# Kernel optimization log

Hardware: AMD Instinct MI355X
Metric: run time of the kernel (lower is better)

The kernel has to match this reference:

```python
import jax, jax.numpy as jnp
import numpy as np

S, D, H, HD = 3072, 1280, 16, 80
FF = 4 * D
EPS = 1e-6


def layernorm(x, scale, bias):
    mu = jnp.mean(x, axis=-1, keepdims=True)
    var = jnp.mean(jnp.square(x - mu), axis=-1, keepdims=True)
    return (x - mu) * jax.lax.rsqrt(var + EPS) * scale + bias


def rotate_half(x):
    x1 = x[..., : x.shape[-1] // 2]
    x2 = x[..., x.shape[-1] // 2 :]
    return jnp.concatenate([-x2, x1], axis=-1)


def apply_rope(x, freqs):
    # x: (S,H,hd), freqs: (S,hd/2)
    cos = jnp.repeat(jnp.cos(freqs), 2, axis=-1)[:, None, :]  # (S,1,hd)
    sin = jnp.repeat(jnp.sin(freqs), 2, axis=-1)[:, None, :]
    return x * cos + rotate_half(x) * sin


def quick_gelu(x):
    return x * jax.nn.sigmoid(1.702 * x)


def setup_inputs() -> dict:
    key = jax.random.key(0)
    ks = jax.random.split(key, 12)
    s = 0.02
    return {
        "hidden_states": jax.random.normal(ks[0], (S, D), jnp.float32),
        "rotary_pos_emb": jax.random.normal(ks[1], (S, HD // 2), jnp.float32),
        "ln1_scale": jnp.ones((D,), jnp.float32),
        "ln1_bias": jnp.zeros((D,), jnp.float32),
        "ln2_scale": jnp.ones((D,), jnp.float32),
        "ln2_bias": jnp.zeros((D,), jnp.float32),
        "qkv_w": jax.random.normal(ks[2], (D, 3 * D), jnp.float32) * s,
        "qkv_b": jnp.zeros((3 * D,), jnp.float32),
        "proj_w": jax.random.normal(ks[3], (D, D), jnp.float32) * s,
        "proj_b": jnp.zeros((D,), jnp.float32),
        "fc1_w": jax.random.normal(ks[4], (D, FF), jnp.float32) * s,
        "fc1_b": jnp.zeros((FF,), jnp.float32),
        "fc2_w": jax.random.normal(ks[5], (FF, D), jnp.float32) * s,
        "fc2_b": jnp.zeros((D,), jnp.float32),
        "cu_seqlens": jnp.array([0, 1024, 2048, 3072], jnp.int32),
    }


def reference(hidden_states, rotary_pos_emb, ln1_scale, ln1_bias, ln2_scale,
              ln2_bias, qkv_w, qkv_b, proj_w, proj_b, fc1_w, fc1_b, fc2_w,
              fc2_b, cu_seqlens):
    x = hidden_states  # (S, D)
    h = layernorm(x, ln1_scale, ln1_bias)
    qkv = (h @ qkv_w + qkv_b).reshape(S, 3, H, HD)
    q, k, v = qkv[:, 0], qkv[:, 1], qkv[:, 2]  # each (S, H, hd)
    q = apply_rope(q, rotary_pos_emb)
    k = apply_rope(k, rotary_pos_emb)

    # block-diagonal varlen mask from cu_seqlens (same segment attends)
    ids = jnp.arange(S)
    seg = jnp.searchsorted(cu_seqlens, ids, side="right")  # (S,)
    valid = seg[:, None] == seg[None, :]  # (S, S)
    bias = jnp.where(valid, 0.0, jnp.finfo(q.dtype).min)

    scale = 1.0 / jnp.sqrt(jnp.asarray(HD, q.dtype))
    scores = jnp.einsum("qhd,khd->hqk", q, k) * scale + bias
    probs = jax.nn.softmax(scores.astype(jnp.float32), axis=-1).astype(q.dtype)
    attn = jnp.einsum("hqk,khd->qhd", probs, v).reshape(S, D)
    attn = attn @ proj_w + proj_b

    x = x + attn
    h2 = layernorm(x, ln2_scale, ln2_bias)
    mlp = quick_gelu(h2 @ fc1_w + fc1_b) @ fc2_w + fc2_b
    return x + mlp
```

## Files before the change

### kernel.cpp

```cpp
#include <hip/hip_runtime.h>

typedef __bf16 bf16x8 __attribute__((ext_vector_type(8)));
typedef float f32x4 __attribute__((ext_vector_type(4)));
typedef unsigned short u16;
typedef u16 u16x4 __attribute__((ext_vector_type(4)));
typedef u16 u16x8 __attribute__((ext_vector_type(8)));
typedef float float4v __attribute__((ext_vector_type(4)));

__device__ __forceinline__ u16 f2bf(float f) {
    __bf16 b = (__bf16)f;
    return __builtin_bit_cast(unsigned short, b);
}
__device__ __forceinline__ float bf2f(u16 x) {
    __bf16 b = __builtin_bit_cast(__bf16, x);
    return (float)b;
}

__device__ __forceinline__ void gld16(const void* g, void* l) {
    __builtin_amdgcn_global_load_lds((const __attribute__((address_space(1))) void*)g,
                                     (__attribute__((address_space(3))) void*)l, 16, 0, 0);
}

__device__ __forceinline__ int xcd_swz(int orig, int nwg) {
    const int q = nwg >> 3, r = nwg & 7;
    const int xcd = orig & 7, pos = orig >> 3;
    return (xcd < r ? xcd * (q + 1) : r * (q + 1) + (xcd - r) * q) + pos;
}

__global__ __launch_bounds__(256) void transpose_all_kernel(
    const float* __restrict__ qkvw, const float* __restrict__ projw,
    const float* __restrict__ fc1w, const float* __restrict__ fc2w,
    u16* __restrict__ qkvwT, u16* __restrict__ projwT,
    u16* __restrict__ fc1wT, u16* __restrict__ fc2wT)
{
    __shared__ u16 tile[64][65];
    int bid = blockIdx.x;
    const float* W; u16* WT; int K, N, nx;
    if (bid < 1200)      { W = qkvw;  WT = qkvwT;  K = 1280; N = 3840; nx = 60; }
    else if (bid < 1600) { bid -= 1200; W = projw; WT = projwT; K = 1280; N = 1280; nx = 20; }
    else if (bid < 3200) { bid -= 1600; W = fc1w;  WT = fc1wT;  K = 1280; N = 5120; nx = 80; }
    else                 { bid -= 3200; W = fc2w;  WT = fc2wT;  K = 5120; N = 1280; nx = 20; }
    const int tx = threadIdx.x & 63, ty = threadIdx.x >> 6;
    const int n0 = (bid % nx) * 64, k0 = (bid / nx) * 64;
    #pragma unroll
    for (int i = ty; i < 64; i += 4)
        tile[i][tx] = f2bf(W[(size_t)(k0 + i) * N + n0 + tx]);
    __syncthreads();
    #pragma unroll
    for (int i = ty; i < 64; i += 4)
        WT[(size_t)(n0 + i) * K + k0 + tx] = tile[tx][i];
}

__global__ __launch_bounds__(256) void ln_kernel(
    const float* __restrict__ x, const float* __restrict__ sc,
    const float* __restrict__ bias, u16* __restrict__ out)
{
    const int row = blockIdx.x, t = threadIdx.x;
    const float* xr = x + (size_t)row * 1280;
    float v[5], s1 = 0.f, s2 = 0.f;
    #pragma unroll
    for (int i = 0; i < 5; i++) {
        v[i] = xr[t + i * 256];
        s1 += v[i];
        s2 += v[i] * v[i];
    }
    #pragma unroll
    for (int off = 32; off; off >>= 1) {
        s1 += __shfl_down(s1, off);
        s2 += __shfl_down(s2, off);
    }
    __shared__ float rA[4], rB[4];
    if ((t & 63) == 0) { rA[t >> 6] = s1; rB[t >> 6] = s2; }
    __syncthreads();
    s1 = rA[0] + rA[1] + rA[2] + rA[3];
    s2 = rB[0] + rB[1] + rB[2] + rB[3];
    const float mu = s1 * (1.f / 1280.f);
    const float var = s2 * (1.f / 1280.f) - mu * mu;
    const float rstd = rsqrtf(var + 1e-6f);
    #pragma unroll
    for (int i = 0; i < 5; i++) {
        const int d = t + i * 256;
        out[(size_t)row * 1280 + d] = f2bf((v[i] - mu) * rstd * sc[d] + bias[d]);
    }
}

__global__ __launch_bounds__(256) void reduce4_ln_kernel(
    const u16* __restrict__ parts, const float* __restrict__ bias,
    const float* __restrict__ res, const float* __restrict__ lns,
    const float* __restrict__ lnb, float* __restrict__ xmid,
    u16* __restrict__ h2, size_t MN)
{
    const int row = blockIdx.x, t = threadIdx.x;
    float v[5], s1 = 0.f, s2 = 0.f;
    #pragma unroll
    for (int i = 0; i < 5; i++) {
        const int d = t + i * 256;
        const size_t idx = (size_t)row * 1280 + d;
        float a = bf2f(parts[idx]) + bf2f(parts[MN + idx])
                + bf2f(parts[2 * MN + idx]) + bf2f(parts[3 * MN + idx])
                + res[idx] + bias[d];
        v[i] = a;
        xmid[idx] = a;
        s1 += a;
        s2 += a * a;
    }
    #pragma unroll
    for (int off = 32; off; off >>= 1) {
        s1 += __shfl_down(s1, off);
        s2 += __shfl_down(s2, off);
    }
    __shared__ float rA[4], rB[4];
    if ((t & 63) == 0) { rA[t >> 6] = s1; rB[t >> 6] = s2; }
    __syncthreads();
    s1 = rA[0] + rA[1] + rA[2] + rA[3];
    s2 = rB[0] + rB[1] + rB[2] + rB[3];
    const float mu = s1 * (1.f / 1280.f);
    const float var = s2 * (1.f / 1280.f) - mu * mu;
    const float rstd = rsqrtf(var + 1e-6f);
    #pragma unroll
    for (int i = 0; i < 5; i++) {
        const int d = t + i * 256;
        h2[(size_t)row * 1280 + d] = f2bf((v[i] - mu) * rstd * lns[d] + lnb[d]);
    }
}

__global__ __launch_bounds__(256) void reduce4b_kernel(
    const u16* __restrict__ parts, const float* __restrict__ bias,
    const float* __restrict__ res, float* __restrict__ out, int N, size_t MN)
{
    const size_t i4 = ((size_t)blockIdx.x * 256 + threadIdx.x) * 4;
    if (i4 >= MN) return;
    float4v a = *reinterpret_cast<const float4v*>(res + i4);
    #pragma unroll
    for (int p = 0; p < 4; p++) {
        u16x4 v = *reinterpret_cast<const u16x4*>(parts + p * MN + i4);
        #pragma unroll
        for (int r = 0; r < 4; r++) a[r] += bf2f(v[r]);
    }
    const int col = (int)(i4 % N);
    a += *reinterpret_cast<const float4v*>(bias + col);
    *reinterpret_cast<float4v*>(out + i4) = a;
}

template <int GELU, int OUTB, int SPLIT>
__global__ __launch_bounds__(512, 2) void gemm256_kernel(
    const u16* __restrict__ A, const u16* __restrict__ BT,
    const float* __restrict__ bias,
    float* __restrict__ outF, u16* __restrict__ outB,
    int M, int N, int K)
{
    __shared__ u16 As[2][256 * 64];
    __shared__ u16 Bs[2][256 * 64];
    const int tid = threadIdx.x, lane = tid & 63, wave = tid >> 6;
    const int nwg = gridDim.x * gridDim.y;
    const int bid = xcd_swz(blockIdx.y * gridDim.x + blockIdx.x, nwg);
    const int m0 = (bid / gridDim.x) * 256, n0 = (bid % gridDim.x) * 256;
    const int wr = wave >> 2, wc = wave & 3;
    const int wm = wr * 128, wn = wc * 64;
    const int lr = lane & 15, lh = lane >> 4;
    const int xa = lr & 7;

    const int kchunk = K / SPLIT;
    const int kz = (SPLIT > 1) ? blockIdx.z : 0;
    const int kbeg = kz * kchunk;
    const int niter = kchunk >> 7;

    const int sr = lane >> 3;
    const int sc8 = (lane & 7) ^ sr;

    f32x4 acc[8][4] = {};
    bf16x8 bq[4][2];

    const char* aRd[2] = {
        (const char*)As + (wm + lr) * 128 + ((0 + lh) ^ xa) * 16,
        (const char*)As + (wm + lr) * 128 + ((4 + lh) ^ xa) * 16 };
    const char* bRd[2] = {
        (const char*)Bs + (wn + lr) * 128 + ((0 + lh) ^ xa) * 16,
        (const char*)Bs + (wn + lr) * 128 + ((4 + lh) ^ xa) * 16 };

    const u16 *aG[2][2], *bG[2][2];
    #pragma unroll
    for (int h = 0; h < 2; h++)
        #pragma unroll
        for (int j = 0; j < 2; j++) {
            const int row = h * 128 + j * 64 + wave * 8 + sr;
            aG[h][j] = A + (size_t)(m0 + row) * K + kbeg + sc8 * 8;
            bG[h][j] = BT + (size_t)(n0 + row) * K + kbeg + sc8 * 8;
        }

    auto stgA = [&](int t, int h) {
        u16* d = (u16*)As + (t & 1) * 16384 + h * 8192 + wave * 512;
        gld16(aG[h][0] + (size_t)t * 64, d);
        gld16(aG[h][1] + (size_t)t * 64, d + 4096);
    };
    auto stgB = [&](int t, int h) {
        u16* d = (u16*)Bs + (t & 1) * 16384 + h * 8192 + wave * 512;
        gld16(bG[h][0] + (size_t)t * 64, d);
        gld16(bG[h][1] + (size_t)t * 64, d + 4096);
    };

#define PHASE(BUF, Q, STGSTMT, VMSTMT)                                          \
    {                                                                           \
        if ((Q) == 0) {                                                         \
            _Pragma("unroll") for (int ni = 0; ni < 4; ni++)                    \
                _Pragma("unroll") for (int kk = 0; kk < 2; kk++)                \
                    bq[ni][kk] = *reinterpret_cast<const bf16x8*>(              \
                        bRd[kk] + (BUF) * 32768 + ni * 2048);                   \
        }                                                                       \
        bf16x8 afq[2][2];                                                       \
        _Pragma("unroll") for (int m2 = 0; m2 < 2; m2++)                        \
            _Pragma("unroll") for (int kk = 0; kk < 2; kk++)                    \
                afq[m2][kk] = *reinterpret_cast<const bf16x8*>(                 \
                    aRd[kk] + (BUF) * 32768 + (Q) * 4096 + m2 * 2048);          \
        VMSTMT;                                                                 \
        __builtin_amdgcn_s_barrier();                                           \
        asm volatile("s_waitcnt lgkmcnt(0)" ::: "memory");                      \
        __builtin_amdgcn_s_setprio(1);                                          \
        _Pragma("unroll") for (int kk = 0; kk < 2; kk++)                        \
            _Pragma("unroll") for (int m2 = 0; m2 < 2; m2++)                    \
                _Pragma("unroll") for (int ni = 0; ni < 4; ni++)                \
                    acc[(Q) * 2 + m2][ni] =                                     \
                        __builtin_amdgcn_mfma_f32_16x16x32_bf16(                \
                            afq[m2][kk], bq[ni][kk], acc[(Q) * 2 + m2][ni],     \
                            0, 0, 0);                                           \
        __builtin_amdgcn_s_setprio(0);                                          \
        STGSTMT;                                                                \
    }

    stgB(0, 0); stgB(0, 1);
    stgA(0, 0); stgA(0, 1);
    stgB(1, 0); stgB(1, 1);
    asm volatile("s_waitcnt vmcnt(4)" ::: "memory");
    __builtin_amdgcn_s_barrier();

    for (int i = 0; i < niter - 1; i++) {
        const int t0 = 2 * i, t1 = 2 * i + 1;
        PHASE(0, 0, stgA(t1, 0), (void)0);
        PHASE(0, 1, stgA(t1, 1), (void)0);
        PHASE(0, 2, stgB(t0 + 2, 0), (void)0);
        PHASE(0, 3, stgB(t0 + 2, 1),
              asm volatile("s_waitcnt vmcnt(2)" ::: "memory"));
        PHASE(1, 0, stgA(t0 + 2, 0), (void)0);
        PHASE(1, 1, stgA(t0 + 2, 1), (void)0);
        PHASE(1, 2, stgB(t1 + 2, 0), (void)0);
        PHASE(1, 3, stgB(t1 + 2, 1),
              asm volatile("s_waitcnt vmcnt(2)" ::: "memory"));
    }
    {
        const int t1 = 2 * niter - 1;
        PHASE(0, 0, stgA(t1, 0), (void)0);
        PHASE(0, 1, stgA(t1, 1), (void)0);
        PHASE(0, 2, (void)0, (void)0);
        PHASE(0, 3, (void)0,
              asm volatile("s_waitcnt vmcnt(0)" ::: "memory"));
        PHASE(1, 0, (void)0, (void)0);
        PHASE(1, 1, (void)0, (void)0);
        PHASE(1, 2, (void)0, (void)0);
        PHASE(1, 3, (void)0, (void)0);
    }
#undef PHASE

    if (SPLIT > 1) {
        u16* pf = outB + (size_t)kz * M * N;
        #pragma unroll
        for (int mi = 0; mi < 8; mi++)
            #pragma unroll
            for (int ni = 0; ni < 4; ni++) {
                const int col = n0 + wn + ni * 16 + lr;
                #pragma unroll
                for (int r = 0; r < 4; r++) {
                    const int rowg = m0 + wm + mi * 16 + lh * 4 + r;
                    pf[(size_t)rowg * N + col] = f2bf(acc[mi][ni][r]);
                }
            }
        return;
    }

    #pragma unroll
    for (int mi = 0; mi < 8; mi++) {
        #pragma unroll
        for (int ni = 0; ni < 4; ni++) {
            const int col = n0 + wn + ni * 16 + lr;
            const float bv = bias[col];
            #pragma unroll
            for (int r = 0; r < 4; r++) {
                const int rowg = m0 + wm + mi * 16 + lh * 4 + r;
                float v = acc[mi][ni][r] + bv;
                if (GELU) v = v * (1.0f / (1.0f + __expf(-1.702f * v)));
                if (OUTB) outB[(size_t)rowg * N + col] = f2bf(v);
            }
        }
    }
}

template <int SPLIT>
__global__ __launch_bounds__(256) void gemm_kernel(
    const u16* __restrict__ A, const u16* __restrict__ BT,
    u16* __restrict__ partB, int M, int N, int K)
{
    __shared__ u16 As[128 * 64];
    __shared__ u16 Bs[128 * 64];
    const int tid = threadIdx.x, lane = tid & 63, wave = tid >> 6;
    const int nwg = gridDim.x * gridDim.y;
    const int bid = xcd_swz(blockIdx.y * gridDim.x + blockIdx.x, nwg);
    const int m0 = (bid / gridDim.x) * 128, n0 = (bid % gridDim.x) * 128;
    const int wm = (wave >> 1) * 64, wn = (wave & 1) * 64;
    const int lr = lane & 15, lh = lane >> 4;
    const int xa = lr & 7;
    const int srow = lane >> 3;
    const int schunk = (lane & 7) ^ (srow & 7);

    const int kchunk = K / SPLIT;
    const int kz = (SPLIT > 1) ? blockIdx.z : 0;
    const int kbeg = kz * kchunk;

    const u16 *aG[4], *bG[4];
    u16 *dA[4], *dB[4];
    #pragma unroll
    for (int s = 0; s < 4; s++) {
        const int seg = wave + s * 4;
        const int row = seg * 8 + srow;
        aG[s] = A + (size_t)(m0 + row) * K + kbeg + schunk * 8;
        bG[s] = BT + (size_t)(n0 + row) * K + kbeg + schunk * 8;
        dA[s] = As + seg * 512;
        dB[s] = Bs + seg * 512;
    }
    const char* aRd[2] = {
        (const char*)As + (wm + lr) * 128 + ((0 + lh) ^ xa) * 16,
        (const char*)As + (wm + lr) * 128 + ((4 + lh) ^ xa) * 16 };
    const char* bRd[2] = {
        (const char*)Bs + (wn + lr) * 128 + ((0 + lh) ^ xa) * 16,
        (const char*)Bs + (wn + lr) * 128 + ((4 + lh) ^ xa) * 16 };

    f32x4 acc[4][4] = {};

    for (int ko = 0; ko < kchunk; ko += 64) {
        #pragma unroll
        for (int s = 0; s < 4; s++) {
            gld16(aG[s] + ko, dA[s]);
            gld16(bG[s] + ko, dB[s]);
        }
        asm volatile("s_waitcnt vmcnt(0)" ::: "memory");
        __syncthreads();

        bf16x8 af[4][2], bfr[4][2];
        #pragma unroll
        for (int mi = 0; mi < 4; mi++)
            #pragma unroll
            for (int kk = 0; kk < 2; kk++)
                af[mi][kk] = *reinterpret_cast<const bf16x8*>(aRd[kk] + mi * 2048);
        #pragma unroll
        for (int ni = 0; ni < 4; ni++)
            #pragma unroll
            for (int kk = 0; kk < 2; kk++)
                bfr[ni][kk] = *reinterpret_cast<const bf16x8*>(bRd[kk] + ni * 2048);
        #pragma unroll
        for (int kk = 0; kk < 2; kk++)
            #pragma unroll
            for (int mi = 0; mi < 4; mi++)
                #pragma unroll
                for (int ni = 0; ni < 4; ni++)
                    acc[mi][ni] = __builtin_amdgcn_mfma_f32_16x16x32_bf16(
                        af[mi][kk], bfr[ni][kk], acc[mi][ni], 0, 0, 0);
        __syncthreads();
    }

    u16* pf = partB + (size_t)kz * M * N;
    #pragma unroll
    for (int mi = 0; mi < 4; mi++)
        #pragma unroll
        for (int ni = 0; ni < 4; ni++) {
            const int col = n0 + wn + ni * 16 + lr;
            #pragma unroll
            for (int r = 0; r < 4; r++) {
                const int rowg = m0 + wm + mi * 16 + lh * 4 + r;
                pf[(size_t)rowg * N + col] = f2bf(acc[mi][ni][r]);
            }
        }
}

__global__ __launch_bounds__(256) void rope_kernel(
    const u16* __restrict__ qkv, const float* __restrict__ freqs,
    u16* __restrict__ qp, u16* __restrict__ kp, u16* __restrict__ vt)
{
    const int s = blockIdx.x, t = threadIdx.x;
    const float scale = 0.1118033988749895f;
    __shared__ float cs[40], sn[40];
    if (t < 40) {
        const float f = freqs[(size_t)s * 40 + t];
        cs[t] = cosf(f);
        sn[t] = sinf(f);
    }
    __syncthreads();
    const u16* row = qkv + (size_t)s * 3840;
    for (int i = t; i < 1280; i += 256) {
        const int h = i / 80, d = i % 80;
        const float c = cs[d >> 1], sv = sn[d >> 1];
        const float q0 = bf2f(row[i]);
        const float q1 = (d < 40) ? -bf2f(row[i + 40]) : bf2f(row[i - 40]);
        qp[((size_t)h * 3072 + s) * 96 + d] = f2bf((q0 * c + q1 * sv) * scale);
        const float k0 = bf2f(row[1280 + i]);
        const float k1 = (d < 40) ? -bf2f(row[1280 + i + 40]) : bf2f(row[1280 + i - 40]);
        kp[((size_t)h * 3072 + s) * 128 + d] = f2bf(k0 * c + k1 * sv);
        vt[((size_t)h * 80 + d) * 3072 + s] = row[2560 + i];
    }
    {
        const int h = t / 16, d = 80 + (t % 16);
        qp[((size_t)h * 3072 + s) * 96 + d] = 0;
    }
    for (int i = t; i < 768; i += 256) {
        const int h = i / 48, d = 80 + (i % 48);
        kp[((size_t)h * 3072 + s) * 128 + d] = 0;
    }
}

__global__ __launch_bounds__(256) void attn_kernel(
    const u16* __restrict__ qp, const u16* __restrict__ kp,
    const u16* __restrict__ vt, u16* __restrict__ attn_out)
{
    const int tid = threadIdx.x, lane = tid & 63, wave = tid >> 6;
    const int w = xcd_swz(blockIdx.x, 768);
    const int qt = w & 15;
    const int h = (w >> 4) & 15;
    const int sq = w >> 8;
    const int lr = lane & 15, lh = lane >> 4;
    const int xa = lr & 7;
    const int qrow = sq * 1024 + qt * 64 + wave * 16;

    __shared__ u16 Ks[2][64 * 128];
    __shared__ u16 Vs[2][80 * 64];

    bf16x8 aq[3];
    {
        const u16* qb = qp + ((size_t)h * 3072 + qrow + lr) * 96 + lh * 8;
        #pragma unroll
        for (int d0 = 0; d0 < 3; d0++)
            aq[d0] = *reinterpret_cast<const bf16x8*>(qb + d0 * 32);
    }

    float m = -1e30f, l = 0.f;
    f32x4 acc[5] = {};

    const u16* kseg = kp + ((size_t)h * 3072 + sq * 1024) * 128;
    const u16* vseg = vt + (size_t)h * 80 * 3072 + sq * 1024;

    const int krow_l = lane >> 4;
    const int kch    = lane & 15;
    const int vrow_l = lane >> 3;
    const int vch    = lane & 7;

    const u16 *kG[4], *vG[3];
    u16 *kD[4], *vD[3];
    #pragma unroll
    for (int s = 0; s < 4; s++) {
        const int seg = wave + s * 4;
        const int row = seg * 4 + krow_l;
        kG[s] = kseg + (size_t)row * 128 + ((kch ^ (row & 7)) * 8);
        kD[s] = (u16*)Ks + seg * 512;
    }
    #pragma unroll
    for (int s = 0; s < 3; s++) {
        const int seg = wave + s * 4;
        const int row = (seg < 10) ? seg * 8 + vrow_l : 0;
        vG[s] = vseg + (size_t)row * 3072 + ((vch ^ (row & 7)) * 8);
        vD[s] = (u16*)Vs + seg * 512;
    }

    auto stageK = [&](int t, int buf) {
        #pragma unroll
        for (int s = 0; s < 4; s++)
            gld16(kG[s] + (size_t)t * 8192, kD[s] + buf * 8192);
    };
    auto stageV = [&](int t, int buf) {
        #pragma unroll
        for (int s = 0; s < 3; s++)
            if (wave + s * 4 < 10)
                gld16(vG[s] + t * 64, vD[s] + buf * 5120);
    };

    stageK(0, 0);
    stageV(0, 0);
    asm volatile("s_waitcnt vmcnt(0)" ::: "memory");
    __syncthreads();

    const char* kRd[3] = {
        (const char*)Ks + lr * 256 + ((0 + lh) ^ xa) * 16,
        (const char*)Ks + lr * 256 + ((4 + lh) ^ xa) * 16,
        (const char*)Ks + lr * 256 + ((8 + lh) ^ xa) * 16 };
    const char* vRd[2] = {
        (const char*)Vs + lr * 128 + ((0 + lh) ^ xa) * 16,
        (const char*)Vs + lr * 128 + ((4 + lh) ^ xa) * 16 };

    const int prow = wave * 16 + lr;
    const int psw = prow & 7;
    const char* pBase = (const char*)Ks + prow * 256;
    const int prd = ((12 + lh) ^ psw) << 4;

    for (int t = 0; t < 16; t++) {
        const int cur = t & 1;
        const int curK = cur * 16384, curV = cur * 10240;
        if (t < 15) {
            stageK(t + 1, cur ^ 1);
            stageV(t + 1, cur ^ 1);
        }

        f32x4 sc[4] = {};
        #pragma unroll
        for (int c = 0; c < 4; c++) {
            #pragma unroll
            for (int d0 = 0; d0 < 3; d0++) {
                bf16x8 kf = *reinterpret_cast<const bf16x8*>(kRd[d0] + curK + c * 4096);
                sc[c] = __builtin_amdgcn_mfma_f32_16x16x32_bf16(kf, aq[d0], sc[c], 0, 0, 0);
            }
        }

        float pmax = sc[0][0];
        #pragma unroll
        for (int c = 0; c < 4; c++)
            #pragma unroll
            for (int r = 0; r < 4; r++)
                pmax = fmaxf(pmax, sc[c][r]);
        pmax = fmaxf(pmax, __shfl_xor(pmax, 16));
        pmax = fmaxf(pmax, __shfl_xor(pmax, 32));

        if (!__all(pmax - m <= 8.0f)) {
            const float mn = fmaxf(m, pmax);
            const float fac = __expf(m - mn);
            m = mn;
            l *= fac;
            #pragma unroll
            for (int df = 0; df < 5; df++)
                #pragma unroll
                for (int r = 0; r < 4; r++)
                    acc[df][r] *= fac;
        }

        float p[4][4], rs = 0.f;
        #pragma unroll
        for (int c = 0; c < 4; c++)
            #pragma unroll
            for (int r = 0; r < 4; r++) {
                p[c][r] = __expf(sc[c][r] - m);
                rs += p[c][r];
            }
        rs += __shfl_xor(rs, 16);
        rs += __shfl_xor(rs, 32);
        l += rs;

        char* pb = (char*)pBase + curK;

        #pragma unroll
        for (int cc = 0; cc < 2; cc++) {
            u16x4 pw;
            #pragma unroll
            for (int r = 0; r < 4; r++)
                pw[r] = f2bf(p[cc][r]);
            *reinterpret_cast<u16x4*>(
                pb + (((12 + cc * 2 + (lh >> 1)) ^ psw) << 4) + (lh & 1) * 8) = pw;
        }
        asm volatile("s_waitcnt lgkmcnt(0)" ::: "memory");
        {
            bf16x8 pa = *reinterpret_cast<const bf16x8*>(pb + prd);
            asm volatile("s_waitcnt lgkmcnt(0)" ::: "memory");
            #pragma unroll
            for (int df = 0; df < 5; df++) {
                bf16x8 vf = *reinterpret_cast<const bf16x8*>(vRd[0] + curV + df * 2048);
                acc[df] = __builtin_amdgcn_mfma_f32_16x16x32_bf16(vf, pa, acc[df], 0, 0, 0);
            }
        }
        #pragma unroll
        for (int cc = 0; cc < 2; cc++) {
            u16x4 pw;
            #pragma unroll
            for (int r = 0; r < 4; r++)
                pw[r] = f2bf(p[2 + cc][r]);
            *reinterpret_cast<u16x4*>(
                pb + (((12 + cc * 2 + (lh >> 1)) ^ psw) << 4) + (lh & 1) * 8) = pw;
        }
        asm volatile("s_waitcnt lgkmcnt(0)" ::: "memory");
        {
            bf16x8 pa = *reinterpret_cast<const bf16x8*>(pb + prd);
            #pragma unroll
            for (int df = 0; df < 5; df++) {
                bf16x8 vf = *reinterpret_cast<const bf16x8*>(vRd[1] + curV + df * 2048);
                acc[df] = __builtin_amdgcn_mfma_f32_16x16x32_bf16(vf, pa, acc[df], 0, 0, 0);
            }
        }

        asm volatile("s_waitcnt vmcnt(0)" ::: "memory");
        __syncthreads();
    }

    const float invl = 1.0f / l;
    u16* orow = attn_out + (size_t)(qrow + lr) * 1280 + h * 80;
    #pragma unroll
    for (int df = 0; df < 5; df++) {
        u16x4 o;
        #pragma unroll
        for (int r = 0; r < 4; r++)
            o[r] = f2bf(acc[df][r] * invl);
        *reinterpret_cast<u16x4*>(orow + df * 16 + lh * 4) = o;
    }
}

extern "C" void kernel_launch(void* const* d_in, const int* in_sizes, int n_in,
                              void* d_out, int out_size, void* d_ws, size_t ws_size,
                              hipStream_t stream) {
    const float* hidden = (const float*)d_in[0];
    const float* rot    = (const float*)d_in[1];
    const float* ln1s   = (const float*)d_in[2];
    const float* ln1b   = (const float*)d_in[3];
    const float* ln2s   = (const float*)d_in[4];
    const float* ln2b   = (const float*)d_in[5];
    const float* qkvw   = (const float*)d_in[6];
    const float* qkvb   = (const float*)d_in[7];
    const float* projw  = (const float*)d_in[8];
    const float* projb  = (const float*)d_in[9];
    const float* fc1w   = (const float*)d_in[10];
    const float* fc1b   = (const float*)d_in[11];
    const float* fc2w   = (const float*)d_in[12];
    const float* fc2b   = (const float*)d_in[13];
    float* out = (float*)d_out;

    char* p = (char*)d_ws;
    auto alloc = [&](size_t n) { char* r = p; p += (n + 255) & ~(size_t)255; return r; };
    u16* qkvwT  = (u16*)alloc((size_t)3840 * 1280 * 2);
    u16* projwT = (u16*)alloc((size_t)1280 * 1280 * 2);
    u16* fc1wT  = (u16*)alloc((size_t)5120 * 1280 * 2);
    u16* fc2wT  = (u16*)alloc((size_t)1280 * 5120 * 2);
    u16* hbuf   = (u16*)alloc((size_t)3072 * 1280 * 2);
    u16* qkvbf  = (u16*)alloc((size_t)3072 * 5120 * 2);
    u16* attnb  = (u16*)alloc((size_t)3072 * 1280 * 2);
    float* xmid = (float*)alloc((size_t)3072 * 1280 * 4);
    u16* partsB = (u16*)alloc((size_t)4 * 3072 * 1280 * 2);
    u16* qp2 = partsB;
    u16* kp2 = qp2 + (size_t)16 * 3072 * 96;
    u16* vt2 = kp2 + (size_t)16 * 3072 * 128;
    u16* h2   = hbuf;
    u16* mlp1 = qkvbf;
    const size_t MN = (size_t)3072 * 1280;

    transpose_all_kernel<<<4800, 256, 0, stream>>>(
        qkvw, projw, fc1w, fc2w, qkvwT, projwT, fc1wT, fc2wT);

    ln_kernel<<<3072, 256, 0, stream>>>(hidden, ln1s, ln1b, hbuf);
    gemm256_kernel<0, 1, 1><<<dim3(15, 12), 512, 0, stream>>>(
        hbuf, qkvwT, qkvb, nullptr, qkvbf, 3072, 3840, 1280);
    rope_kernel<<<3072, 256, 0, stream>>>(qkvbf, rot, qp2, kp2, vt2);
    attn_kernel<<<768, 256, 0, stream>>>(qp2, kp2, vt2, attnb);
    gemm_kernel<4><<<dim3(10, 24, 4), 256, 0, stream>>>(
        attnb, projwT, partsB, 3072, 1280, 1280);
    reduce4_ln_kernel<<<3072, 256, 0, stream>>>(
        partsB, projb, hidden, ln2s, ln2b, xmid, h2, MN);
    gemm256_kernel<1, 1, 1><<<dim3(20, 12), 512, 0, stream>>>(
        h2, fc1wT, fc1b, nullptr, mlp1, 3072, 5120, 1280);
    gemm256_kernel<0, 0, 4><<<dim3(5, 12, 4), 512, 0, stream>>>(
        mlp1, fc2wT, fc2b, nullptr, partsB, 3072, 1280, 5120);
    reduce4b_kernel<<<(int)(MN / 4 / 256), 256, 0, stream>>>(partsB, fc2b, xmid, out, 1280, MN);
}
```

Measured before the change: 279.3 us.

## Add 256x128 GEMM kernel with higher occupancy for QKV and FC2

Introduces a new GEMM kernel using 256x128 tiles and a K-step of 32 with smaller LDS buffers, allowing four blocks per CU, and switches the QKV projection and the split-K FC2 GEMM to it. Smaller tiles double the grid size (180→360 and 240→480 blocks), which is meant to cut wave-quantization and tail underuse on the 256-CU device. In exchange it adds more global traffic per FLOP, more syncs per K (half-size K steps), and uses scalar u16 epilogue stores.

```diff
diff --git a/kernel.cpp b/kernel.cpp
--- a/kernel.cpp
+++ b/kernel.cpp
@@ -140,6 +140,106 @@
     const int col = (int)(i4 % N);
     a += *reinterpret_cast<const float4v*>(bias + col);
     *reinterpret_cast<float4v*>(out + i4) = a;
+}
+
+template <int GELU, int OUTB, int SPLIT>
+__global__ __launch_bounds__(512, 4) void gemm_mn_kernel(
+    const u16* __restrict__ A, const u16* __restrict__ BT,
+    const float* __restrict__ bias,
+    u16* __restrict__ outB, int M, int N, int K)
+{
+    __shared__ u16 As[2][256 * 32];
+    __shared__ u16 Bs[2][128 * 32];
+    const int tid = threadIdx.x, lane = tid & 63, wave = tid >> 6;
+    const int nwg = gridDim.x * gridDim.y;
+    const int bid = xcd_swz(blockIdx.y * gridDim.x + blockIdx.x, nwg);
+    const int m0 = (bid / gridDim.x) * 256, n0 = (bid % gridDim.x) * 128;
+    const int wm = (wave >> 1) * 64, wn = (wave & 1) * 64;
+    const int lr = lane & 15, lh = lane >> 4;
+
+    const int kchunk = K / SPLIT;
+    const int kz = (SPLIT > 1) ? blockIdx.z : 0;
+    const int kbeg = kz * kchunk;
+    const int nt = kchunk >> 5;
+
+    const int sr4 = lane >> 2, sch = lane & 3;
+
+    const int rowA0 = wave * 32 + sr4;
+    const int rowB  = wave * 16 + sr4;
+    const u16* aG0 = A + (size_t)(m0 + rowA0) * K + kbeg + (sch ^ ((rowA0 >> 1) & 3)) * 8;
+    const u16* aG1 = A + (size_t)(m0 + rowA0 + 16) * K + kbeg + (sch ^ (((rowA0 + 16) >> 1) & 3)) * 8;
+    const u16* bG  = BT + (size_t)(n0 + rowB) * K + kbeg + (sch ^ ((rowB >> 1) & 3)) * 8;
+
+    auto stage = [&](int t, int buf) {
+        u16* da = (u16*)As + buf * 8192 + wave * 1024;
+        gld16(aG0 + t * 32, da);
+        gld16(aG1 + t * 32, da + 512);
+        gld16(bG + t * 32, (u16*)Bs + buf * 4096 + wave * 512);
+    };
+
+    const int xsw = (lh ^ ((lr >> 1) & 3)) * 16;
+    const char* aRd = (const char*)As + (wm + lr) * 64 + xsw;
+    const char* bRd = (const char*)Bs + (wn + lr) * 64 + xsw;
+
+    f32x4 acc[4][4] = {};
+
+    stage(0, 0);
+    __syncthreads();
+
+    for (int t = 0; t < nt; t++) {
+        const int buf = t & 1;
+        if (t + 1 < nt) stage(t + 1, buf ^ 1);
+
+        bf16x8 af[4], bf[4];
+        #pragma unroll
+        for (int mi = 0; mi < 4; mi++)
+            af[mi] = *reinterpret_cast<const bf16x8*>(aRd + buf * 16384 + mi * 1024);
+        #pragma unroll
+        for (int ni = 0; ni < 4; ni++)
+            bf[ni] = *reinterpret_cast<const bf16x8*>(bRd + buf * 8192 + ni * 1024);
+
+        __builtin_amdgcn_s_setprio(1);
+        #pragma unroll
+        for (int mi = 0; mi < 4; mi++)
+            #pragma unroll
+            for (int ni = 0; ni < 4; ni++)
+                acc[mi][ni] = __builtin_amdgcn_mfma_f32_16x16x32_bf16(
+                    af[mi], bf[ni], acc[mi][ni], 0, 0, 0);
+        __builtin_amdgcn_s_setprio(0);
+        __syncthreads();
+    }
+
+    if (SPLIT > 1) {
+        u16* pf = outB + (size_t)kz * M * N;
+        #pragma unroll
+        for (int mi = 0; mi < 4; mi++)
+            #pragma unroll
+            for (int ni = 0; ni < 4; ni++) {
+                const int col = n0 + wn + ni * 16 + lr;
+                #pragma unroll
+                for (int r = 0; r < 4; r++) {
+                    const int rowg = m0 + wm + mi * 16 + lh * 4 + r;
+                    pf[(size_t)rowg * N + col] = f2bf(acc[mi][ni][r]);
+                }
+            }
+        return;
+    }
+
+    #pragma unroll
+    for (int mi = 0; mi < 4; mi++) {
+        #pragma unroll
+        for (int ni = 0; ni < 4; ni++) {
+            const int col = n0 + wn + ni * 16 + lr;
+            const float bv = bias[col];
+            #pragma unroll
+            for (int r = 0; r < 4; r++) {
+                const int rowg = m0 + wm + mi * 16 + lh * 4 + r;
+                float v = acc[mi][ni][r] + bv;
+                if (GELU) v = v * (1.0f / (1.0f + __expf(-1.702f * v)));
+                outB[(size_t)rowg * N + col] = f2bf(v);
+            }
+        }
+    }
 }
 
 template <int GELU, int OUTB, int SPLIT>
@@ -644,8 +744,8 @@
         qkvw, projw, fc1w, fc2w, qkvwT, projwT, fc1wT, fc2wT);
 
     ln_kernel<<<3072, 256, 0, stream>>>(hidden, ln1s, ln1b, hbuf);
-    gemm256_kernel<0, 1, 1><<<dim3(15, 12), 512, 0, stream>>>(
-        hbuf, qkvwT, qkvb, nullptr, qkvbf, 3072, 3840, 1280);
+    gemm_mn_kernel<0, 1, 1><<<dim3(30, 12), 512, 0, stream>>>(
+        hbuf, qkvwT, qkvb, qkvbf, 3072, 3840, 1280);
     rope_kernel<<<3072, 256, 0, stream>>>(qkvbf, rot, qp2, kp2, vt2);
     attn_kernel<<<768, 256, 0, stream>>>(qp2, kp2, vt2, attnb);
     gemm_kernel<4><<<dim3(10, 24, 4), 256, 0, stream>>>(
@@ -654,7 +754,7 @@
         partsB, projb, hidden, ln2s, ln2b, xmid, h2, MN);
     gemm256_kernel<1, 1, 1><<<dim3(20, 12), 512, 0, stream>>>(
         h2, fc1wT, fc1b, nullptr, mlp1, 3072, 5120, 1280);
-    gemm256_kernel<0, 0, 4><<<dim3(5, 12, 4), 512, 0, stream>>>(
-        mlp1, fc2wT, fc2b, nullptr, partsB, 3072, 1280, 5120);
+    gemm_mn_kernel<0, 0, 4><<<dim3(10, 12, 4), 512, 0, stream>>>(
+        mlp1, fc2wT, fc2b, partsB, 3072, 1280, 5120);
     reduce4b_kernel<<<(int)(MN / 4 / 256), 256, 0, stream>>>(partsB, fc2b, xmid, out, 1280, MN);
 }
```

After: 281.4 us. About the same (+0.7%).

## Replace shared-tile GEMMs with wave-private LDS staging kernel for all projections

Applied to the files above, without the earlier changes.

Replaces both GEMM kernels with one kernel in which each wave stages its own 64x32 A and B slices into a private LDS region, with no block barriers. The block tile shrinks from 256x256 to 256x128, and occupancy rises to four blocks per SM. This removes cross-wave barrier stalls and the heavy pipelined schedule. In exchange, the waves no longer share tiles, so each wave reloads data the others also need. That means much more global and L2 traffic, smaller K steps, and only single-buffered prefetch.

```diff
diff --git a/kernel.cpp b/kernel.cpp
--- a/kernel.cpp
+++ b/kernel.cpp
@@ -142,128 +142,78 @@
     *reinterpret_cast<float4v*>(out + i4) = a;
 }
 
-template <int GELU, int OUTB, int SPLIT>
-__global__ __launch_bounds__(512, 2) void gemm256_kernel(
+template <int GELU, int SPLIT>
+__global__ __launch_bounds__(512, 4) void gemm_wp_kernel(
     const u16* __restrict__ A, const u16* __restrict__ BT,
     const float* __restrict__ bias,
-    float* __restrict__ outF, u16* __restrict__ outB,
-    int M, int N, int K)
-{
-    __shared__ u16 As[2][256 * 64];
-    __shared__ u16 Bs[2][256 * 64];
+    u16* __restrict__ outB, int M, int N, int K)
+{
+    __shared__ u16 Wl[8][2][2048];
     const int tid = threadIdx.x, lane = tid & 63, wave = tid >> 6;
     const int nwg = gridDim.x * gridDim.y;
     const int bid = xcd_swz(blockIdx.y * gridDim.x + blockIdx.x, nwg);
-    const int m0 = (bid / gridDim.x) * 256, n0 = (bid % gridDim.x) * 256;
-    const int wr = wave >> 2, wc = wave & 3;
-    const int wm = wr * 128, wn = wc * 64;
+    const int m0 = (bid / gridDim.x) * 256, n0 = (bid % gridDim.x) * 128;
+    const int wm = (wave >> 1) * 64, wn = (wave & 1) * 64;
     const int lr = lane & 15, lh = lane >> 4;
-    const int xa = lr & 7;
 
     const int kchunk = K / SPLIT;
     const int kz = (SPLIT > 1) ? blockIdx.z : 0;
     const int kbeg = kz * kchunk;
-    const int niter = kchunk >> 7;
-
-    const int sr = lane >> 3;
-    const int sc8 = (lane & 7) ^ sr;
-
-    f32x4 acc[8][4] = {};
-    bf16x8 bq[4][2];
-
-    const char* aRd[2] = {
-        (const char*)As + (wm + lr) * 128 + ((0 + lh) ^ xa) * 16,
-        (const char*)As + (wm + lr) * 128 + ((4 + lh) ^ xa) * 16 };
-    const char* bRd[2] = {
-        (const char*)Bs + (wn + lr) * 128 + ((0 + lh) ^ xa) * 16,
-        (const char*)Bs + (wn + lr) * 128 + ((4 + lh) ^ xa) * 16 };
-
-    const u16 *aG[2][2], *bG[2][2];
-    #pragma unroll
-    for (int h = 0; h < 2; h++)
-        #pragma unroll
-        for (int j = 0; j < 2; j++) {
-            const int row = h * 128 + j * 64 + wave * 8 + sr;
-            aG[h][j] = A + (size_t)(m0 + row) * K + kbeg + sc8 * 8;
-            bG[h][j] = BT + (size_t)(n0 + row) * K + kbeg + sc8 * 8;
-        }
-
-    auto stgA = [&](int t, int h) {
-        u16* d = (u16*)As + (t & 1) * 16384 + h * 8192 + wave * 512;
-        gld16(aG[h][0] + (size_t)t * 64, d);
-        gld16(aG[h][1] + (size_t)t * 64, d + 4096);
+    const int nt = kchunk >> 5;
+
+    const int sr = lane >> 2, sch8 = (lane & 3) * 8;
+
+    const u16 *aG[4], *bG[4];
+    #pragma unroll
+    for (int j = 0; j < 4; j++) {
+        aG[j] = A + (size_t)(m0 + wm + j * 16 + sr) * K + kbeg + sch8;
+        bG[j] = BT + (size_t)(n0 + wn + j * 16 + sr) * K + kbeg + sch8;
+    }
+    u16* aL = Wl[wave][0];
+    u16* bL = Wl[wave][1];
+
+    auto stage = [&](int t) {
+        #pragma unroll
+        for (int j = 0; j < 4; j++) {
+            gld16(aG[j] + t * 32, aL + j * 512);
+            gld16(bG[j] + t * 32, bL + j * 512);
+        }
     };
-    auto stgB = [&](int t, int h) {
-        u16* d = (u16*)Bs + (t & 1) * 16384 + h * 8192 + wave * 512;
-        gld16(bG[h][0] + (size_t)t * 64, d);
-        gld16(bG[h][1] + (size_t)t * 64, d + 4096);
-    };
-
-#define PHASE(BUF, Q, STGSTMT, VMSTMT)                                          \
-    {                                                                           \
-        if ((Q) == 0) {                                                         \
-            _Pragma("unroll") for (int ni = 0; ni < 4; ni++)                    \
-                _Pragma("unroll") for (int kk = 0; kk < 2; kk++)                \
-                    bq[ni][kk] = *reinterpret_cast<const bf16x8*>(              \
-                        bRd[kk] + (BUF) * 32768 + ni * 2048);                   \
-        }                                                                       \
-        bf16x8 afq[2][2];                                                       \
-        _Pragma("unroll") for (int m2 = 0; m2 < 2; m2++)                        \
-            _Pragma("unroll") for (int kk = 0; kk < 2; kk++)                    \
-                afq[m2][kk] = *reinterpret_cast<const bf16x8*>(                 \
-                    aRd[kk] + (BUF) * 32768 + (Q) * 4096 + m2 * 2048);          \
-        VMSTMT;                                                                 \
-        __builtin_amdgcn_s_barrier();                                           \
-        asm volatile("s_waitcnt lgkmcnt(0)" ::: "memory");                      \
-        __builtin_amdgcn_s_setprio(1);                                          \
-        _Pragma("unroll") for (int kk = 0; kk < 2; kk++)                        \
-            _Pragma("unroll") for (int m2 = 0; m2 < 2; m2++)                    \
-                _Pragma("unroll") for (int ni = 0; ni < 4; ni++)                \
-                    acc[(Q) * 2 + m2][ni] =                                     \
-                        __builtin_amdgcn_mfma_f32_16x16x32_bf16(                \
-                            afq[m2][kk], bq[ni][kk], acc[(Q) * 2 + m2][ni],     \
-                            0, 0, 0);                                           \
-        __builtin_amdgcn_s_setprio(0);                                          \
-        STGSTMT;                                                                \
-    }
-
-    stgB(0, 0); stgB(0, 1);
-    stgA(0, 0); stgA(0, 1);
-    stgB(1, 0); stgB(1, 1);
-    asm volatile("s_waitcnt vmcnt(4)" ::: "memory");
-    __builtin_amdgcn_s_barrier();
-
-    for (int i = 0; i < niter - 1; i++) {
-        const int t0 = 2 * i, t1 = 2 * i + 1;
-        PHASE(0, 0, stgA(t1, 0), (void)0);
-        PHASE(0, 1, stgA(t1, 1), (void)0);
-        PHASE(0, 2, stgB(t0 + 2, 0), (void)0);
-        PHASE(0, 3, stgB(t0 + 2, 1),
-              asm volatile("s_waitcnt vmcnt(2)" ::: "memory"));
-        PHASE(1, 0, stgA(t0 + 2, 0), (void)0);
-        PHASE(1, 1, stgA(t0 + 2, 1), (void)0);
-        PHASE(1, 2, stgB(t1 + 2, 0), (void)0);
-        PHASE(1, 3, stgB(t1 + 2, 1),
-              asm volatile("s_waitcnt vmcnt(2)" ::: "memory"));
-    }
-    {
-        const int t1 = 2 * niter - 1;
-        PHASE(0, 0, stgA(t1, 0), (void)0);
-        PHASE(0, 1, stgA(t1, 1), (void)0);
-        PHASE(0, 2, (void)0, (void)0);
-        PHASE(0, 3, (void)0,
-              asm volatile("s_waitcnt vmcnt(0)" ::: "memory"));
-        PHASE(1, 0, (void)0, (void)0);
-        PHASE(1, 1, (void)0, (void)0);
-        PHASE(1, 2, (void)0, (void)0);
-        PHASE(1, 3, (void)0, (void)0);
-    }
-#undef PHASE
+
+    const char* aRd = (const char*)aL + lr * 64 + lh * 16;
+    const char* bRd = (const char*)bL + lr * 64 + lh * 16;
+
+    f32x4 acc[4][4] = {};
+
+    stage(0);
+
+    for (int t = 0; t < nt; t++) {
+        asm volatile("s_waitcnt vmcnt(0)" ::: "memory");
+        bf16x8 af[4], bf[4];
+        #pragma unroll
+        for (int mi = 0; mi < 4; mi++)
+            af[mi] = *reinterpret_cast<const bf16x8*>(aRd + mi * 1024);
+        #pragma unroll
+        for (int ni = 0; ni < 4; ni++)
+            bf[ni] = *reinterpret_cast<const bf16x8*>(bRd + ni * 1024);
+        asm volatile("s_waitcnt lgkmcnt(0)" ::: "memory");
+        __builtin_amdgcn_sched_barrier(0);
+        if (t + 1 < nt) stage(t + 1);
+
+        __builtin_amdgcn_s_setprio(1);
+        #pragma unroll
+        for (int mi = 0; mi < 4; mi++)
+            #pragma unroll
+            for (int ni = 0; ni < 4; ni++)
+                acc[mi][ni] = __builtin_amdgcn_mfma_f32_16x16x32_bf16(
+                    af[mi], bf[ni], acc[mi][ni], 0, 0, 0);
+        __builtin_amdgcn_s_setprio(0);
+    }
 
     if (SPLIT > 1) {
         u16* pf = outB + (size_t)kz * M * N;
         #pragma unroll
-        for (int mi = 0; mi < 8; mi++)
+        for (int mi = 0; mi < 4; mi++)
             #pragma unroll
             for (int ni = 0; ni < 4; ni++) {
                 const int col = n0 + wn + ni * 16 + lr;
@@ -277,7 +227,7 @@
     }
 
     #pragma unroll
-    for (int mi = 0; mi < 8; mi++) {
+    for (int mi = 0; mi < 4; mi++) {
         #pragma unroll
         for (int ni = 0; ni < 4; ni++) {
             const int col = n0 + wn + ni * 16 + lr;
@@ -287,96 +237,10 @@
                 const int rowg = m0 + wm + mi * 16 + lh * 4 + r;
                 float v = acc[mi][ni][r] + bv;
                 if (GELU) v = v * (1.0f / (1.0f + __expf(-1.702f * v)));
-                if (OUTB) outB[(size_t)rowg * N + col] = f2bf(v);
+                outB[(size_t)rowg * N + col] = f2bf(v);
             }
         }
     }
-}
-
-template <int SPLIT>
-__global__ __launch_bounds__(256) void gemm_kernel(
-    const u16* __restrict__ A, const u16* __restrict__ BT,
-    u16* __restrict__ partB, int M, int N, int K)
-{
-    __shared__ u16 As[128 * 64];
-    __shared__ u16 Bs[128 * 64];
-    const int tid = threadIdx.x, lane = tid & 63, wave = tid >> 6;
-    const int nwg = gridDim.x * gridDim.y;
-    const int bid = xcd_swz(blockIdx.y * gridDim.x + blockIdx.x, nwg);
-    const int m0 = (bid / gridDim.x) * 128, n0 = (bid % gridDim.x) * 128;
-    const int wm = (wave >> 1) * 64, wn = (wave & 1) * 64;
-    const int lr = lane & 15, lh = lane >> 4;
-    const int xa = lr & 7;
-    const int srow = lane >> 3;
-    const int schunk = (lane & 7) ^ (srow & 7);
-
-    const int kchunk = K / SPLIT;
-    const int kz = (SPLIT > 1) ? blockIdx.z : 0;
-    const int kbeg = kz * kchunk;
-
-    const u16 *aG[4], *bG[4];
-    u16 *dA[4], *dB[4];
-    #pragma unroll
-    for (int s = 0; s < 4; s++) {
-        const int seg = wave + s * 4;
-        const int row = seg * 8 + srow;
-        aG[s] = A + (size_t)(m0 + row) * K + kbeg + schunk * 8;
-        bG[s] = BT + (size_t)(n0 + row) * K + kbeg + schunk * 8;
-        dA[s] = As + seg * 512;
-        dB[s] = Bs + seg * 512;
-    }
-    const char* aRd[2] = {
-        (const char*)As + (wm + lr) * 128 + ((0 + lh) ^ xa) * 16,
-        (const char*)As + (wm + lr) * 128 + ((4 + lh) ^ xa) * 16 };
-    const char* bRd[2] = {
-        (const char*)Bs + (wn + lr) * 128 + ((0 + lh) ^ xa) * 16,
-        (const char*)Bs + (wn + lr) * 128 + ((4 + lh) ^ xa) * 16 };
-
-    f32x4 acc[4][4] = {};
-
-    for (int ko = 0; ko < kchunk; ko += 64) {
-        #pragma unroll
-        for (int s = 0; s < 4; s++) {
-            gld16(aG[s] + ko, dA[s]);
-            gld16(bG[s] + ko, dB[s]);
-        }
-        asm volatile("s_waitcnt vmcnt(0)" ::: "memory");
-        __syncthreads();
-
-        bf16x8 af[4][2], bfr[4][2];
-        #pragma unroll
-        for (int mi = 0; mi < 4; mi++)
-            #pragma unroll
-            for (int kk = 0; kk < 2; kk++)
-                af[mi][kk] = *reinterpret_cast<const bf16x8*>(aRd[kk] + mi * 2048);
-        #pragma unroll
-        for (int ni = 0; ni < 4; ni++)
-            #pragma unroll
-            for (int kk = 0; kk < 2; kk++)
-                bfr[ni][kk] = *reinterpret_cast<const bf16x8*>(bRd[kk] + ni * 2048);
-        #pragma unroll
-        for (int kk = 0; kk < 2; kk++)
-            #pragma unroll
-            for (int mi = 0; mi < 4; mi++)
-                #pragma unroll
-                for (int ni = 0; ni < 4; ni++)
-                    acc[mi][ni] = __builtin_amdgcn_mfma_f32_16x16x32_bf16(
-                        af[mi][kk], bfr[ni][kk], acc[mi][ni], 0, 0, 0);
-        __syncthreads();
-    }
-
-    u16* pf = partB + (size_t)kz * M * N;
-    #pragma unroll
-    for (int mi = 0; mi < 4; mi++)
-        #pragma unroll
-        for (int ni = 0; ni < 4; ni++) {
-            const int col = n0 + wn + ni * 16 + lr;
-            #pragma unroll
-            for (int r = 0; r < 4; r++) {
-                const int rowg = m0 + wm + mi * 16 + lh * 4 + r;
-                pf[(size_t)rowg * N + col] = f2bf(acc[mi][ni][r]);
-            }
-        }
 }
 
 __global__ __launch_bounds__(256) void rope_kernel(
@@ -644,17 +508,17 @@
         qkvw, projw, fc1w, fc2w, qkvwT, projwT, fc1wT, fc2wT);
 
     ln_kernel<<<3072, 256, 0, stream>>>(hidden, ln1s, ln1b, hbuf);
-    gemm256_kernel<0, 1, 1><<<dim3(15, 12), 512, 0, stream>>>(
-        hbuf, qkvwT, qkvb, nullptr, qkvbf, 3072, 3840, 1280);
+    gemm_wp_kernel<0, 1><<<dim3(30, 12), 512, 0, stream>>>(
+        hbuf, qkvwT, qkvb, qkvbf, 3072, 3840, 1280);
     rope_kernel<<<3072, 256, 0, stream>>>(qkvbf, rot, qp2, kp2, vt2);
     attn_kernel<<<768, 256, 0, stream>>>(qp2, kp2, vt2, attnb);
-    gemm_kernel<4><<<dim3(10, 24, 4), 256, 0, stream>>>(
-        attnb, projwT, partsB, 3072, 1280, 1280);
+    gemm_wp_kernel<0, 4><<<dim3(10, 12, 4), 512, 0, stream>>>(
+        attnb, projwT, projb, partsB, 3072, 1280, 1280);
     reduce4_ln_kernel<<<3072, 256, 0, stream>>>(
         partsB, projb, hidden, ln2s, ln2b, xmid, h2, MN);
-    gemm256_kernel<1, 1, 1><<<dim3(20, 12), 512, 0, stream>>>(
-        h2, fc1wT, fc1b, nullptr, mlp1, 3072, 5120, 1280);
-    gemm256_kernel<0, 0, 4><<<dim3(5, 12, 4), 512, 0, stream>>>(
-        mlp1, fc2wT, fc2b, nullptr, partsB, 3072, 1280, 5120);
+    gemm_wp_kernel<1, 1><<<dim3(40, 12), 512, 0, stream>>>(
+        h2, fc1wT, fc1b, mlp1, 3072, 5120, 1280);
+    gemm_wp_kernel<0, 4><<<dim3(10, 12, 4), 512, 0, stream>>>(
+        mlp1, fc2wT, fc2b, partsB, 3072, 1280, 5120);
     reduce4b_kernel<<<(int)(MN / 4 / 256), 256, 0, stream>>>(partsB, fc2b, xmid, out, 1280, MN);
 }
```

New measurement: 413.4 us. 48.0% more time.
